# Performance work log

Hardware: AMD Instinct MI355X
Metric: run time of the kernel (lower is better)

Reference implementation:

```python
import jax, jax.numpy as jnp
import numpy as np

DIM = 256
NUM_HEADS = 8
HEAD_DIM = DIM // NUM_HEADS          # 32
KEY_DIM = int(HEAD_DIM * 0.5)        # 16
SCALE = KEY_DIM ** (-0.5)
QKV_OUT = DIM + 2 * KEY_DIM * NUM_HEADS  # 512
BN_EPS = 1e-3


def _bn(x, gamma, beta, mean, var):
    # inference-mode BatchNorm2d over channel axis 1 of NCHW
    inv = gamma / jnp.sqrt(var + BN_EPS)
    return x * inv[None, :, None, None] + (beta - mean * inv)[None, :, None, None]


def _conv1x1(x, w):
    # w: (O, C, 1, 1)
    return jnp.einsum('bchw,oc->bohw', x, w[:, :, 0, 0])


def _dwconv3x3(x, w):
    # depthwise 3x3, SAME padding; w: (C, 1, 3, 3)
    return jax.lax.conv_general_dilated(
        x, w, window_strides=(1, 1), padding='SAME',
        feature_group_count=x.shape[1],
        dimension_numbers=('NCHW', 'OIHW', 'NCHW'))


def setup_inputs() -> dict:
    key = jax.random.key(0)
    ks = jax.random.split(key, 16)
    B, C, H, W = 16, DIM, 32, 32
    inp = {
        'x': jax.random.normal(ks[0], (B, C, H, W), jnp.float32),
        'qkv_w': jax.random.normal(ks[1], (QKV_OUT, DIM, 1, 1), jnp.float32) * (1.0 / np.sqrt(DIM)),
        'qkv_gamma': jnp.ones((QKV_OUT,), jnp.float32),
        'qkv_beta': jnp.zeros((QKV_OUT,), jnp.float32),
        'qkv_mean': jax.random.normal(ks[2], (QKV_OUT,), jnp.float32) * 0.1,
        'qkv_var': jax.random.uniform(ks[3], (QKV_OUT,), jnp.float32, 0.5, 1.5),
        'pe_w': jax.random.normal(ks[4], (DIM, 1, 3, 3), jnp.float32) * (1.0 / 3.0),
        'pe_gamma': jnp.ones((DIM,), jnp.float32),
        'pe_beta': jnp.zeros((DIM,), jnp.float32),
        'pe_mean': jax.random.normal(ks[5], (DIM,), jnp.float32) * 0.1,
        'pe_var': jax.random.uniform(ks[6], (DIM,), jnp.float32, 0.5, 1.5),
        'proj_w': jax.random.normal(ks[7], (DIM, DIM, 1, 1), jnp.float32) * (1.0 / np.sqrt(DIM)),
        'proj_gamma': jnp.ones((DIM,), jnp.float32),
        'proj_beta': jnp.zeros((DIM,), jnp.float32),
        'proj_mean': jax.random.normal(ks[8], (DIM,), jnp.float32) * 0.1,
        'proj_var': jax.random.uniform(ks[9], (DIM,), jnp.float32, 0.5, 1.5),
    }
    return inp


def reference(x, qkv_w, qkv_gamma, qkv_beta, qkv_mean, qkv_var,
              pe_w, pe_gamma, pe_beta, pe_mean, pe_var,
              proj_w, proj_gamma, proj_beta, proj_mean, proj_var):
    B, C, H, W = x.shape
    N = H * W
    # qkv: 1x1 conv + BN (act=False)
    qkv = _bn(_conv1x1(x, qkv_w), qkv_gamma, qkv_beta, qkv_mean, qkv_var)
    qkv = qkv.reshape(B, NUM_HEADS, 2 * KEY_DIM + HEAD_DIM, N)
    q = qkv[:, :, :KEY_DIM]                          # (B, h, kd, N)
    k = qkv[:, :, KEY_DIM:2 * KEY_DIM]               # (B, h, kd, N)
    v = qkv[:, :, 2 * KEY_DIM:]                      # (B, h, hd, N)
    # attn = (q^T @ k) * scale, softmax over last dim
    attn = jnp.einsum('bhdn,bhdm->bhnm', q, k) * SCALE   # (B, h, N, N)
    attn = jax.nn.softmax(attn, axis=-1)
    # v @ attn^T
    v_attn = jnp.einsum('bhdn,bhmn->bhdm', v, attn)      # (B, h, hd, N)
    v_attn = v_attn.reshape(B, C, H, W)
    v_reshaped = v.reshape(B, C, H, W)
    pos_enc = _bn(_dwconv3x3(v_reshaped, pe_w), pe_gamma, pe_beta, pe_mean, pe_var)
    out = v_attn + pos_enc
    out = _bn(_conv1x1(out, proj_w), proj_gamma, proj_beta, proj_mean, proj_var)
    return out
```

## Files before the change

### kernel.cpp

```cpp
#include <hip/hip_runtime.h>

#define B_ 16
#define C_ 256
#define N_ 1024
#define NH 8
#define HD 32
#define KD 16
#define QKV_OUT_ 512
#define BN_EPS 1e-3f
#define SCALE2_ (0.25f * 1.44269504088896f)

typedef __attribute__((ext_vector_type(8))) short short8;
typedef __attribute__((ext_vector_type(16))) float float16;

__device__ inline unsigned short f2bf(float f) {
  unsigned int u = __float_as_uint(f);
  return (unsigned short)((u + 0x7FFF + ((u >> 16) & 1)) >> 16);
}
__device__ inline float bf2f(unsigned short s) {
  return __uint_as_float(((unsigned int)s) << 16);
}
__device__ inline float16 zero16() {
  float16 z;
  #pragma unroll
  for (int i = 0; i < 16; ++i) z[i] = 0.f;
  return z;
}
__device__ inline unsigned int pack_bf16_trunc(float a, float b) {
  return __builtin_amdgcn_perm(__float_as_uint(b), __float_as_uint(a), 0x07060302u);
}
__device__ inline unsigned int pack_bf16_rne(float a, float b) {
  return (unsigned int)f2bf(a) | ((unsigned int)f2bf(b) << 16);
}
__device__ inline float fast_exp2(float x) {
#if __has_builtin(__builtin_amdgcn_exp2f)
  return __builtin_amdgcn_exp2f(x);
#else
  return exp2f(x);
#endif
}
__device__ inline void pl32(unsigned int& a, unsigned int& b) {
#if __has_builtin(__builtin_amdgcn_permlane32_swap)
  typedef __attribute__((ext_vector_type(2))) int int2v;
  int2v r = __builtin_amdgcn_permlane32_swap((int)a, (int)b, false, false);
  a = (unsigned int)r[0];
  b = (unsigned int)r[1];
#else
  unsigned int ea = (unsigned int)__shfl_xor((int)a, 32, 64);
  unsigned int eb = (unsigned int)__shfl_xor((int)b, 32, 64);
  bool hi = (threadIdx.x & 32) != 0;
  unsigned int an = hi ? eb : a;
  unsigned int bn = hi ? b : ea;
  a = an; b = bn;
#endif
}
__device__ inline short8 lds_frag(const unsigned short* p) {
  union { uint2 u[2]; short8 s; } r;
  r.u[0] = *(const uint2*)p;
  r.u[1] = *(const uint2*)(p + 4);
  return r.s;
}
__device__ inline void lds_store16(unsigned short* p, uint4 v) {
  *(uint2*)p = make_uint2(v.x, v.y);
  *(uint2*)(p + 4) = make_uint2(v.z, v.w);
}

__global__ __launch_bounds__(256) void fold_weights(
    const float* __restrict__ qkv_w, const float* __restrict__ qg,
    const float* __restrict__ qb, const float* __restrict__ qm,
    const float* __restrict__ qv,
    const float* __restrict__ proj_w, const float* __restrict__ pg,
    const float* __restrict__ pb, const float* __restrict__ pm,
    const float* __restrict__ pv,
    unsigned short* __restrict__ wq, float* __restrict__ biasq,
    unsigned short* __restrict__ wp, float* __restrict__ biasp)
{
  const int o = blockIdx.x, c = threadIdx.x;
  if (o < QKV_OUT_) {
    float s = ((o & 63) < 16) ? SCALE2_ : 1.f;
    float inv = qg[o] * rsqrtf(qv[o] + BN_EPS) * s;
    wq[o * C_ + c] = f2bf(qkv_w[o * C_ + c] * inv);
    if (c == 0) biasq[o] = qb[o] * s - qm[o] * inv;
  } else {
    int oo = o - QKV_OUT_;
    float inv = pg[oo] * rsqrtf(pv[oo] + BN_EPS);
    wp[oo * C_ + c] = f2bf(proj_w[oo * C_ + c] * inv);
    if (c == 0) biasp[oo] = pb[oo] - pm[oo] * inv;
  }
}

__global__ __launch_bounds__(256) void gemm_qkv(
    const float* __restrict__ x, const unsigned short* __restrict__ wq,
    const float* __restrict__ bias,
    unsigned short* __restrict__ qkT, unsigned short* __restrict__ vbuf)
{
  constexpr int STR = 44;
  __shared__ __align__(8) unsigned short wa[2][128 * STR];
  __shared__ __align__(8) unsigned short xb[2][128 * STR];
  const int tid = threadIdx.x;
  const int wave = tid >> 6, lane = tid & 63, l31 = lane & 31, lh = lane >> 5;
  const int wm = wave & 1, wn = wave >> 1;
  const int b = blockIdx.x >> 3, nloc = (blockIdx.x & 7) * 128;
  const int o0 = blockIdx.y * 128;

  const int r0 = tid >> 2, oc0 = (tid & 3) * 8;
  const int r1 = r0 + 64;
  const int tok = tid & 127, chalf = (tid >> 7) * 16;
  const float* xbase = x + (size_t)b * C_ * N_ + nloc + tok;

  uint4 ga0, ga1;
  float nb[16];

  auto loadk = [&](int kc) {
    ga0 = *(const uint4*)(wq + (size_t)(o0 + r0) * C_ + kc * 32 + oc0);
    ga1 = *(const uint4*)(wq + (size_t)(o0 + r1) * C_ + kc * 32 + oc0);
    #pragma unroll
    for (int j = 0; j < 16; ++j)
      nb[j] = xbase[(size_t)(kc * 32 + chalf + j) * N_];
  };
  auto storek = [&](int bufi) {
    lds_store16(&wa[bufi][r0 * STR + oc0], ga0);
    lds_store16(&wa[bufi][r1 * STR + oc0], ga1);
    unsigned int pk[8];
    #pragma unroll
    for (int q = 0; q < 8; ++q) pk[q] = pack_bf16_rne(nb[2 * q], nb[2 * q + 1]);
    lds_store16(&xb[bufi][tok * STR + chalf], make_uint4(pk[0], pk[1], pk[2], pk[3]));
    lds_store16(&xb[bufi][tok * STR + chalf + 8], make_uint4(pk[4], pk[5], pk[6], pk[7]));
  };

  float16 acc[2][2];
  #pragma unroll
  for (int i = 0; i < 2; ++i)
    #pragma unroll
    for (int j = 0; j < 2; ++j) acc[i][j] = zero16();

  loadk(0);
  storek(0);
  __syncthreads();

  for (int kc = 0; kc < 8; ++kc) {
    const int buf = kc & 1;
    if (kc < 7) loadk(kc + 1);

    #pragma unroll
    for (int ks = 0; ks < 2; ++ks) {
      const int ko = ks * 16 + lh * 8;
      short8 a0 = lds_frag(&wa[buf][(wm * 64 + l31) * STR + ko]);
      short8 a1 = lds_frag(&wa[buf][(wm * 64 + 32 + l31) * STR + ko]);
      short8 b0 = lds_frag(&xb[buf][(wn * 64 + l31) * STR + ko]);
      short8 b1 = lds_frag(&xb[buf][(wn * 64 + 32 + l31) * STR + ko]);
      acc[0][0] = __builtin_amdgcn_mfma_f32_32x32x16_bf16(a0, b0, acc[0][0], 0, 0, 0);
      acc[0][1] = __builtin_amdgcn_mfma_f32_32x32x16_bf16(a0, b1, acc[0][1], 0, 0, 0);
      acc[1][0] = __builtin_amdgcn_mfma_f32_32x32x16_bf16(a1, b0, acc[1][0], 0, 0, 0);
      acc[1][1] = __builtin_amdgcn_mfma_f32_32x32x16_bf16(a1, b1, acc[1][1], 0, 0, 0);
    }

    if (kc < 7) storek(buf ^ 1);
    __syncthreads();
  }

  const int hh = (o0 >> 6) + wm;
  #pragma unroll
  for (int bn = 0; bn < 2; ++bn) {
    int n = nloc + wn * 64 + bn * 32 + l31;
    unsigned short* row = qkT + (((size_t)b * NH + hh) * N_ + n) * 32;
    #pragma unroll
    for (int qd = 0; qd < 4; ++qd) {
      int cc0 = 8 * qd + 4 * lh;
      ushort4 rv;
      rv.x = f2bf(acc[0][bn][4 * qd + 0] + bias[hh * 64 + cc0 + 0]);
      rv.y = f2bf(acc[0][bn][4 * qd + 1] + bias[hh * 64 + cc0 + 1]);
      rv.z = f2bf(acc[0][bn][4 * qd + 2] + bias[hh * 64 + cc0 + 2]);
      rv.w = f2bf(acc[0][bn][4 * qd + 3] + bias[hh * 64 + cc0 + 3]);
      *(ushort4*)(row + cc0) = rv;
    }
  }
  #pragma unroll
  for (int r = 0; r < 16; ++r) {
    int d = (r & 3) + 8 * (r >> 2) + 4 * lh;
    float bo = bias[hh * 64 + 32 + d];
    unsigned short* vrow =
        vbuf + ((size_t)b * C_ + hh * 32 + d) * N_ + nloc + wn * 64 + l31;
    #pragma unroll
    for (int bn = 0; bn < 2; ++bn)
      vrow[bn * 32] = f2bf(acc[1][bn][r] + bo);
  }
}

__global__ __launch_bounds__(256) void gemm_proj(
    const unsigned short* __restrict__ inT, const unsigned short* __restrict__ wp,
    const float* __restrict__ bias, float* __restrict__ outf)
{
  constexpr int STR = 44;
  __shared__ __align__(8) unsigned short wa[2][64 * STR];
  __shared__ __align__(8) unsigned short xb[2][128 * STR];
  const int tid = threadIdx.x;
  const int wave = tid >> 6, lane = tid & 63, l31 = lane & 31, lh = lane >> 5;
  const int wm = wave & 1, wn = wave >> 1;
  const int n0g = blockIdx.x * 128;
  const int o0 = blockIdx.y * 64;
  const int b = n0g >> 10, nloc = n0g & 1023;

  const int ar = tid >> 2, aseg = (tid & 3) * 8;

  float16 acc[2];
  acc[0] = zero16(); acc[1] = zero16();

  uint4 ga, gb0, gb1;
  auto loadk = [&](int kc) {
    ga  = *(const uint4*)(wp + (size_t)(o0 + ar) * C_ + kc * 32 + aseg);
    gb0 = *(const uint4*)(inT + (size_t)(n0g + ar) * C_ + kc * 32 + aseg);
    gb1 = *(const uint4*)(inT + (size_t)(n0g + ar + 64) * C_ + kc * 32 + aseg);
  };
  auto storek = [&](int bufi) {
    lds_store16(&wa[bufi][ar * STR + aseg], ga);
    lds_store16(&xb[bufi][ar * STR + aseg], gb0);
    lds_store16(&xb[bufi][(ar + 64) * STR + aseg], gb1);
  };

  loadk(0);
  storek(0);
  __syncthreads();

  for (int kc = 0; kc < 8; ++kc) {
    const int buf = kc & 1;
    if (kc < 7) loadk(kc + 1);

    #pragma unroll
    for (int ks = 0; ks < 2; ++ks) {
      const int ko = ks * 16 + lh * 8;
      short8 a0 = lds_frag(&wa[buf][(wm * 32 + l31) * STR + ko]);
      short8 b0 = lds_frag(&xb[buf][(wn * 64 + l31) * STR + ko]);
      short8 b1 = lds_frag(&xb[buf][(wn * 64 + 32 + l31) * STR + ko]);
      acc[0] = __builtin_amdgcn_mfma_f32_32x32x16_bf16(a0, b0, acc[0], 0, 0, 0);
      acc[1] = __builtin_amdgcn_mfma_f32_32x32x16_bf16(a0, b1, acc[1], 0, 0, 0);
    }

    if (kc < 7) storek(buf ^ 1);
    __syncthreads();
  }

  #pragma unroll
  for (int r = 0; r < 16; ++r) {
    int o = o0 + wm * 32 + (r & 3) + 8 * (r >> 2) + 4 * lh;
    float bo = bias[o];
    float* orow = outf + ((size_t)b * C_ + o) * N_ + nloc + wn * 64 + l31;
    #pragma unroll
    for (int bn = 0; bn < 2; ++bn)
      orow[bn * 32] = acc[bn][r] + bo;
  }
}

__global__ __launch_bounds__(256) void dwconv_bn(
    const unsigned short* __restrict__ vbuf, const float* __restrict__ pw,
    const float* __restrict__ gamma, const float* __restrict__ beta,
    const float* __restrict__ mean, const float* __restrict__ var,
    unsigned short* __restrict__ posb)
{
  __shared__ float t[34][34];
  const int c = blockIdx.x, b = blockIdx.y;
  const int tid = threadIdx.x;
  const unsigned short* vp = vbuf + ((size_t)b * C_ + c) * N_;

  #pragma unroll
  for (int r = 0; r < 4; ++r) {
    int idx = r * 256 + tid;
    t[(idx >> 5) + 1][(idx & 31) + 1] = bf2f(vp[idx]);
  }
  if (tid < 34) {
    t[0][tid] = 0.f; t[33][tid] = 0.f;
    t[tid][0] = 0.f; t[tid][33] = 0.f;
  }
  __syncthreads();

  float w9[9];
  #pragma unroll
  for (int i = 0; i < 9; ++i) w9[i] = pw[c * 9 + i];
  float inv = gamma[c] * rsqrtf(var[c] + BN_EPS);
  float add = beta[c] - mean[c] * inv;

  unsigned short* op = posb + ((size_t)b * C_ + c) * N_;
  #pragma unroll
  for (int r = 0; r < 4; ++r) {
    int idx = r * 256 + tid;
    int y = idx >> 5, x = idx & 31;
    float s = 0.f;
    #pragma unroll
    for (int dy = 0; dy < 3; ++dy)
      #pragma unroll
      for (int dx = 0; dx < 3; ++dx)
        s += t[y + dy][x + dx] * w9[dy * 3 + dx];
    op[idx] = f2bf(s * inv + add);
  }
}

__global__ __launch_bounds__(256) void attn_mfma(
    const unsigned short* __restrict__ qkT, const unsigned short* __restrict__ vbuf,
    const unsigned short* __restrict__ posb, unsigned short* __restrict__ vattnT)
{
  __shared__ __align__(8) unsigned short k_lds[2][128 * 28];
  __shared__ __align__(8) unsigned short v_lds[2][32 * 140];

  const int tid = threadIdx.x;
  const int wave = tid >> 6, lane = tid & 63;
  const int l31 = lane & 31, lh = lane >> 5;
  const int b = blockIdx.x >> 3, h = blockIdx.x & 7;
  const int qbase = blockIdx.y * 128 + wave * 32;

  const unsigned short* qkb = qkT + ((size_t)b * NH + h) * N_ * 32;
  const unsigned short* vhead = vbuf + ((size_t)b * C_ + h * HD) * N_;

  const int skey = tid >> 1, shalf = tid & 1;
  const int svd = tid >> 3, svseg = tid & 7;

  short8 qf = *(const short8*)(qkb + (size_t)(qbase + l31) * 32 + lh * 8);

  uint4 gk, gv0, gv1;
  auto loadc = [&](int kc) {
    gk  = *(const uint4*)(qkb + (size_t)(kc + skey) * 32 + 16 + shalf * 8);
    gv0 = *(const uint4*)(vhead + (size_t)svd * N_ + kc + svseg * 16);
    gv1 = *(const uint4*)(vhead + (size_t)svd * N_ + kc + svseg * 16 + 8);
  };
  auto storec = [&](int bufi) {
    lds_store16(&k_lds[bufi][skey * 28 + shalf * 8], gk);
    lds_store16(&v_lds[bufi][svd * 140 + svseg * 16], gv0);
    lds_store16(&v_lds[bufi][svd * 140 + svseg * 16 + 8], gv1);
  };

  loadc(0);
  storec(0);
  __syncthreads();

  float16 oaccE = zero16(), oaccO = zero16();
  float ls[4] = {0.f, 0.f, 0.f, 0.f};

  for (int c = 0; c < 8; ++c) {
    const int buf = c & 1;
    if (c < 7) loadc((c + 1) * 128);

    #pragma unroll
    for (int t = 0; t < 4; ++t) {
      const int key0 = t * 32;
      short8 kf = lds_frag(&k_lds[buf][(key0 + l31) * 28 + lh * 8]);
      float16 st = __builtin_amdgcn_mfma_f32_32x32x16_bf16(kf, qf, zero16(), 0, 0, 0);

      unsigned int u[8];
      #pragma unroll
      for (int q = 0; q < 8; ++q) {
        float pe = fast_exp2(st[2 * q]);
        float po = fast_exp2(st[2 * q + 1]);
        ls[q & 3] += pe + po;
        u[q] = pack_bf16_trunc(pe, po);
      }

      #pragma unroll
      for (int f = 0; f < 2; ++f) {
        short8 vf = lds_frag(&v_lds[buf][l31 * 140 + key0 + f * 16 + lh * 8]);
        const int q0 = f * 4;
        unsigned int a0 = u[q0], a2 = u[q0 + 2]; pl32(a0, a2);
        unsigned int a1 = u[q0 + 1], a3 = u[q0 + 3]; pl32(a1, a3);
        union { unsigned int w[4]; short8 s; } bf;
        bf.w[0] = a0; bf.w[1] = a1; bf.w[2] = a2; bf.w[3] = a3;
        if (f == 0)
          oaccE = __builtin_amdgcn_mfma_f32_32x32x16_bf16(vf, bf.s, oaccE, 0, 0, 0);
        else
          oaccO = __builtin_amdgcn_mfma_f32_32x32x16_bf16(vf, bf.s, oaccO, 0, 0, 0);
      }
    }

    if (c < 7) storec(buf ^ 1);
    __syncthreads();
  }

  float lsum = (ls[0] + ls[1]) + (ls[2] + ls[3]);
  lsum += __shfl_xor(lsum, 32, 64);
  const float linv = 1.f / lsum;

  const int token = qbase + l31;
  float val[16];
  #pragma unroll
  for (int r = 0; r < 16; ++r) {
    int d = (r & 3) + 8 * (r >> 2) + 4 * lh;
    val[r] = (oaccE[r] + oaccO[r]) * linv +
             bf2f(posb[((size_t)b * C_ + h * HD + d) * N_ + token]);
  }
  unsigned int u[8];
  #pragma unroll
  for (int m = 0; m < 8; ++m) u[m] = pack_bf16_rne(val[2 * m], val[2 * m + 1]);
  pl32(u[0], u[4]); pl32(u[1], u[5]); pl32(u[2], u[6]); pl32(u[3], u[7]);
  unsigned short* row = vattnT + ((size_t)b * N_ + token) * C_ + h * HD + lh * 16;
  *(uint4*)(row)     = make_uint4(u[0], u[1], u[4], u[5]);
  *(uint4*)(row + 8) = make_uint4(u[2], u[3], u[6], u[7]);
}

extern "C" void kernel_launch(void* const* d_in, const int* in_sizes, int n_in,
                              void* d_out, int out_size, void* d_ws, size_t ws_size,
                              hipStream_t stream) {
  const float* x          = (const float*)d_in[0];
  const float* qkv_w      = (const float*)d_in[1];
  const float* qkv_gamma  = (const float*)d_in[2];
  const float* qkv_beta   = (const float*)d_in[3];
  const float* qkv_mean   = (const float*)d_in[4];
  const float* qkv_var    = (const float*)d_in[5];
  const float* pe_w       = (const float*)d_in[6];
  const float* pe_gamma   = (const float*)d_in[7];
  const float* pe_beta    = (const float*)d_in[8];
  const float* pe_mean    = (const float*)d_in[9];
  const float* pe_var     = (const float*)d_in[10];
  const float* proj_w     = (const float*)d_in[11];
  const float* proj_gamma = (const float*)d_in[12];
  const float* proj_beta  = (const float*)d_in[13];
  const float* proj_mean  = (const float*)d_in[14];
  const float* proj_var   = (const float*)d_in[15];
  float* out = (float*)d_out;

  char* ws = (char*)d_ws;
  unsigned short* qkT = (unsigned short*)ws;
  ws += (size_t)B_ * NH * N_ * 32 * sizeof(unsigned short);
  unsigned short* vbuf = (unsigned short*)ws;
  ws += (size_t)B_ * C_ * N_ * sizeof(unsigned short);
  unsigned short* vattnT = (unsigned short*)ws;
  ws += (size_t)B_ * N_ * C_ * sizeof(unsigned short);
  unsigned short* posb = (unsigned short*)ws;
  ws += (size_t)B_ * C_ * N_ * sizeof(unsigned short);
  unsigned short* wq = (unsigned short*)ws;
  ws += (size_t)QKV_OUT_ * C_ * sizeof(unsigned short);
  unsigned short* wp = (unsigned short*)ws;
  ws += (size_t)C_ * C_ * sizeof(unsigned short);
  float* biasq = (float*)ws; ws += QKV_OUT_ * sizeof(float);
  float* biasp = (float*)ws;

  fold_weights<<<dim3(QKV_OUT_ + C_), 256, 0, stream>>>(
      qkv_w, qkv_gamma, qkv_beta, qkv_mean, qkv_var,
      proj_w, proj_gamma, proj_beta, proj_mean, proj_var,
      wq, biasq, wp, biasp);

  gemm_qkv<<<dim3(128, 4), 256, 0, stream>>>(x, wq, biasq, qkT, vbuf);

  dwconv_bn<<<dim3(C_, B_), 256, 0, stream>>>(
      vbuf, pe_w, pe_gamma, pe_beta, pe_mean, pe_var, posb);

  attn_mfma<<<dim3(128, 8), 256, 0, stream>>>(qkT, vbuf, posb, vattnT);

  gemm_proj<<<dim3(128, 4), 256, 0, stream>>>(vattnT, wp, biasp, out);
}
```

Baseline: 153.8 us.

## Fuse depthwise positional-encoding conv and BN into attention epilogue

Removes the separate dwconv_bn kernel and its bf16 posb intermediate buffer. The 3x3 depthwise conv with folded BN is now computed inside the attention kernel's epilogue, reading V directly from global memory with per-head folded weights staged in reused shared memory. This saves one launch plus a full write and read of the positional-encoding tensor. In exchange the epilogue issues scattered, mostly uncoalesced global loads and recomputes the BN fold in every block.

```diff
diff --git a/kernel.cpp b/kernel.cpp
--- a/kernel.cpp
+++ b/kernel.cpp
@@ -251,55 +251,15 @@
   }
 }
 
-__global__ __launch_bounds__(256) void dwconv_bn(
-    const unsigned short* __restrict__ vbuf, const float* __restrict__ pw,
-    const float* __restrict__ gamma, const float* __restrict__ beta,
-    const float* __restrict__ mean, const float* __restrict__ var,
-    unsigned short* __restrict__ posb)
-{
-  __shared__ float t[34][34];
-  const int c = blockIdx.x, b = blockIdx.y;
-  const int tid = threadIdx.x;
-  const unsigned short* vp = vbuf + ((size_t)b * C_ + c) * N_;
-
-  #pragma unroll
-  for (int r = 0; r < 4; ++r) {
-    int idx = r * 256 + tid;
-    t[(idx >> 5) + 1][(idx & 31) + 1] = bf2f(vp[idx]);
-  }
-  if (tid < 34) {
-    t[0][tid] = 0.f; t[33][tid] = 0.f;
-    t[tid][0] = 0.f; t[tid][33] = 0.f;
-  }
-  __syncthreads();
-
-  float w9[9];
-  #pragma unroll
-  for (int i = 0; i < 9; ++i) w9[i] = pw[c * 9 + i];
-  float inv = gamma[c] * rsqrtf(var[c] + BN_EPS);
-  float add = beta[c] - mean[c] * inv;
-
-  unsigned short* op = posb + ((size_t)b * C_ + c) * N_;
-  #pragma unroll
-  for (int r = 0; r < 4; ++r) {
-    int idx = r * 256 + tid;
-    int y = idx >> 5, x = idx & 31;
-    float s = 0.f;
-    #pragma unroll
-    for (int dy = 0; dy < 3; ++dy)
-      #pragma unroll
-      for (int dx = 0; dx < 3; ++dx)
-        s += t[y + dy][x + dx] * w9[dy * 3 + dx];
-    op[idx] = f2bf(s * inv + add);
-  }
-}
-
 __global__ __launch_bounds__(256) void attn_mfma(
     const unsigned short* __restrict__ qkT, const unsigned short* __restrict__ vbuf,
-    const unsigned short* __restrict__ posb, unsigned short* __restrict__ vattnT)
+    const float* __restrict__ pw, const float* __restrict__ peg,
+    const float* __restrict__ peb, const float* __restrict__ pem,
+    const float* __restrict__ pev, unsigned short* __restrict__ vattnT)
 {
-  __shared__ __align__(8) unsigned short k_lds[2][128 * 28];
-  __shared__ __align__(8) unsigned short v_lds[2][32 * 140];
+  __shared__ __align__(16) unsigned short smem[2 * 128 * 28 + 2 * 32 * 140];
+  unsigned short* kl = smem;
+  unsigned short* vl = smem + 2 * 128 * 28;
 
   const int tid = threadIdx.x;
   const int wave = tid >> 6, lane = tid & 63;
@@ -322,9 +282,9 @@
     gv1 = *(const uint4*)(vhead + (size_t)svd * N_ + kc + svseg * 16 + 8);
   };
   auto storec = [&](int bufi) {
-    lds_store16(&k_lds[bufi][skey * 28 + shalf * 8], gk);
-    lds_store16(&v_lds[bufi][svd * 140 + svseg * 16], gv0);
-    lds_store16(&v_lds[bufi][svd * 140 + svseg * 16 + 8], gv1);
+    lds_store16(kl + bufi * (128 * 28) + skey * 28 + shalf * 8, gk);
+    lds_store16(vl + bufi * (32 * 140) + svd * 140 + svseg * 16, gv0);
+    lds_store16(vl + bufi * (32 * 140) + svd * 140 + svseg * 16 + 8, gv1);
   };
 
   loadc(0);
@@ -341,7 +301,7 @@
     #pragma unroll
     for (int t = 0; t < 4; ++t) {
       const int key0 = t * 32;
-      short8 kf = lds_frag(&k_lds[buf][(key0 + l31) * 28 + lh * 8]);
+      short8 kf = lds_frag(kl + buf * (128 * 28) + (key0 + l31) * 28 + lh * 8);
       float16 st = __builtin_amdgcn_mfma_f32_32x32x16_bf16(kf, qf, zero16(), 0, 0, 0);
 
       unsigned int u[8];
@@ -355,7 +315,7 @@
 
       #pragma unroll
       for (int f = 0; f < 2; ++f) {
-        short8 vf = lds_frag(&v_lds[buf][l31 * 140 + key0 + f * 16 + lh * 8]);
+        short8 vf = lds_frag(vl + buf * (32 * 140) + l31 * 140 + key0 + f * 16 + lh * 8);
         const int q0 = f * 4;
         unsigned int a0 = u[q0], a2 = u[q0 + 2]; pl32(a0, a2);
         unsigned int a1 = u[q0 + 1], a3 = u[q0 + 3]; pl32(a1, a3);
@@ -372,18 +332,51 @@
     __syncthreads();
   }
 
+  float* wlds  = (float*)smem;
+  float* addld = wlds + 288;
+  for (int i = tid; i < 288; i += 256) {
+    int d = i / 9;
+    int cg = h * HD + d;
+    float iv = peg[cg] * rsqrtf(pev[cg] + BN_EPS);
+    wlds[i] = pw[cg * 9 + (i - d * 9)] * iv;
+  }
+  if (tid < 32) {
+    int cg = h * HD + tid;
+    float iv = peg[cg] * rsqrtf(pev[cg] + BN_EPS);
+    addld[tid] = peb[cg] - pem[cg] * iv;
+  }
+  __syncthreads();
+
   float lsum = (ls[0] + ls[1]) + (ls[2] + ls[3]);
   lsum += __shfl_xor(lsum, 32, 64);
   const float linv = 1.f / lsum;
 
   const int token = qbase + l31;
+  const int y = token >> 5;
+  const int x = l31;
+  const bool xm = (x > 0), xp = (x < 31);
+
   float val[16];
   #pragma unroll
   for (int r = 0; r < 16; ++r) {
     int d = (r & 3) + 8 * (r >> 2) + 4 * lh;
-    val[r] = (oaccE[r] + oaccO[r]) * linv +
-             bf2f(posb[((size_t)b * C_ + h * HD + d) * N_ + token]);
-  }
+    const unsigned short* vp = vhead + (size_t)d * N_;
+    const float* wr = wlds + d * 9;
+    float pos = addld[d];
+    #pragma unroll
+    for (int dy = 0; dy < 3; ++dy) {
+      int yy = y + dy - 1;
+      if (yy >= 0 && yy <= 31) {
+        const unsigned short* rp = vp + yy * 32;
+        float c0 = xm ? bf2f(rp[x - 1]) : 0.f;
+        float c1 = bf2f(rp[x]);
+        float c2 = xp ? bf2f(rp[x + 1]) : 0.f;
+        pos += wr[dy * 3 + 0] * c0 + wr[dy * 3 + 1] * c1 + wr[dy * 3 + 2] * c2;
+      }
+    }
+    val[r] = (oaccE[r] + oaccO[r]) * linv + pos;
+  }
+
   unsigned int u[8];
   #pragma unroll
   for (int m = 0; m < 8; ++m) u[m] = pack_bf16_rne(val[2 * m], val[2 * m + 1]);
@@ -421,8 +414,6 @@
   ws += (size_t)B_ * C_ * N_ * sizeof(unsigned short);
   unsigned short* vattnT = (unsigned short*)ws;
   ws += (size_t)B_ * N_ * C_ * sizeof(unsigned short);
-  unsigned short* posb = (unsigned short*)ws;
-  ws += (size_t)B_ * C_ * N_ * sizeof(unsigned short);
   unsigned short* wq = (unsigned short*)ws;
   ws += (size_t)QKV_OUT_ * C_ * sizeof(unsigned short);
   unsigned short* wp = (unsigned short*)ws;
@@ -437,10 +428,8 @@
 
   gemm_qkv<<<dim3(128, 4), 256, 0, stream>>>(x, wq, biasq, qkT, vbuf);
 
-  dwconv_bn<<<dim3(C_, B_), 256, 0, stream>>>(
-      vbuf, pe_w, pe_gamma, pe_beta, pe_mean, pe_var, posb);
-
-  attn_mfma<<<dim3(128, 8), 256, 0, stream>>>(qkT, vbuf, posb, vattnT);
+  attn_mfma<<<dim3(128, 8), 256, 0, stream>>>(
+      qkT, vbuf, pe_w, pe_gamma, pe_beta, pe_mean, pe_var, vattnT);
 
   gemm_proj<<<dim3(128, 4), 256, 0, stream>>>(vattnT, wp, biasp, out);
 }
```

New measurement: 168.2 us. +9.4%, slower.
